# Optimization experiments

Hardware: AMD Instinct MI355X
Metric: run time of the kernel (lower is better)

Reference implementation:

```python
import jax, jax.numpy as jnp
import numpy as np

K_SIGN = 100000.0   # tanh sharpness approximating sign()
EPS = 1e-05         # acos clamp epsilon


def setup_inputs() -> dict:
    key = jax.random.key(0)
    B, N, KV = 2, 8, 64
    contour = jax.random.uniform(key, (B, N, KV, 2), dtype=jnp.float32)  # values in [0,1]
    return {"contour": contour, "size": 128}


def reference(contour, size):
    b, n, kv, _ = contour.shape
    dt = contour.dtype
    # pixel grid, normalized by size (matches torch meshgrid 'ij' + reshape(-1,2)/size)
    g = jnp.arange(size, dtype=dt)
    mesh = jnp.stack(jnp.meshgrid(g, g, indexing="ij"), axis=-1).reshape(-1, 2) / size  # (S2, 2)

    c = contour.reshape(b * n, 1, kv, 2)          # (bn, 1, kv, 2)
    diff = c - mesh[None, :, None, :]             # (bn, S2, kv, 2)
    roll_diff = jnp.roll(diff, -1, axis=2)        # next vertex

    # sign = diff * swap(roll_diff); sign[...,1]-sign[...,0] = d_y*rd_x - d_x*rd_y
    cross = diff[..., 1] * roll_diff[..., 0] - diff[..., 0] * roll_diff[..., 1]
    sign = jnp.tanh(K_SIGN * cross)               # (bn, S2, kv)

    norm_diff = jnp.linalg.norm(diff, axis=3)
    norm_roll = jnp.linalg.norm(roll_diff, axis=3)
    scalar = jnp.sum(diff * roll_diff, axis=3)
    cosang = jnp.clip(scalar / (norm_diff * norm_roll), -1.0 + EPS, 1.0 - EPS)
    angles = jnp.arccos(cosang)                   # (bn, S2, kv)

    sum_angles = jnp.clip(jnp.abs(jnp.sum(sign * angles, axis=2) / (2.0 * jnp.pi)), 0.0, 1.0)
    return sum_angles.reshape(b, n, size, size)
```

## Files before the change

kernel.cpp:

```cpp
#include <hip/hip_runtime.h>
#include <math.h>

#define BLOCK 256
#define SPLIT 4
#define PPT   2
#define MAX_KV_LDS 1024

__device__ __forceinline__ float rcp1(float x)  { return __builtin_amdgcn_rcpf(x); }
__device__ __forceinline__ float rsq1(float x)  { return __builtin_amdgcn_rsqf(x); }
__device__ __forceinline__ float sqrt1(float x) { return __builtin_amdgcn_sqrtf(x); }

__device__ __forceinline__ float edge_term_s(float cr, float dt)
{
    float n2 = fmaf(cr, cr, dt * dt);
    float co = dt * rsq1(n2);
    co = __builtin_amdgcn_fmed3f(co, -0.99999f, 0.99999f);
    float y = fabsf(co);
    float p = fmaf(fmaf(fmaf(-0.0187293f, y, 0.0742610f), y, -0.2121144f),
                   y, 1.5707288f);
    float a = sqrt1(1.0f - y) * p;
    a = (co >= 0.0f) ? a : (3.14159265358979f - a);
    float t  = cr * 100000.0f;
    float s  = t * t;
    float nm = t * fmaf(s + 105.0f, s, 945.0f);
    float qd = fmaf(fmaf(15.0f, s, 420.0f), s, 945.0f);
    float th = __builtin_amdgcn_fmed3f(nm * rcp1(qd), -1.0f, 1.0f);
    return th * a;
}

__global__ __launch_bounds__(BLOCK, 8)
void contour_mask_kernel(const float2* __restrict__ contour,
                         const int* __restrict__ size_ptr,
                         float* __restrict__ out,
                         int out_size, int in0_elems)
{
    __shared__ float2 verts[MAX_KV_LDS + 1];

    const int size     = *size_ptr;
    const int S2       = size * size;
    const int bn_total = out_size / S2;
    const int kv       = in0_elems / (bn_total * 2);

    const int tid  = threadIdx.x;
    const int PIX_PER_BLOCK = (BLOCK / SPLIT) * PPT;
    const int base = blockIdx.x * PIX_PER_BLOCK;

    const int bn0 = base / S2;
    const int rem = base - bn0 * S2;
    const bool one_image = (rem + PIX_PER_BLOCK <= S2) &&
                           (base + PIX_PER_BLOCK <= out_size);
    const bool use_lds = (kv <= MAX_KV_LDS) && one_image;

    if (use_lds) {
        for (int i = tid; i < kv; i += BLOCK)
            verts[i] = contour[(size_t)bn0 * kv + i];
        if (tid == 0)
            verts[kv] = contour[(size_t)bn0 * kv];
    }
    __syncthreads();

    const int seg = tid & (SPLIT - 1);
    const float inv_size = 1.0f / (float)size;
    const float INV2PI = 0.15915494309189535f;

    if (use_lds && kv == 64 && (size & 1) == 0) {
        const int pi0 = rem / size;
        const int pj0 = rem - pi0 * size;
        const int t   = (tid / SPLIT) * PPT;

        int pjA = pj0 + t, piA = pi0;
        while (pjA >= size) { pjA -= size; ++piA; }

        const float mx  = (float)piA * inv_size;
        const float myA = (float)pjA * inv_size;

        const int k0 = seg * 16;
        float2 v = verts[k0];
        float dx  = v.x - mx;
        float dyA = v.y - myA;
        float dyB = dyA - inv_size;
        float accA = 0.0f, accB = 0.0f;

        #pragma unroll
        for (int k = 0; k < 16; ++k) {
            float2 vn = verts[k0 + k + 1];
            float rx  = vn.x - mx;
            float ryA = vn.y - myA;
            float ryB = ryA - inv_size;
            float P   = dx * rx;
            float dtA = fmaf(dyA, ryA, P);
            float dtB = fmaf(dyB, ryB, P);
            float crA = fmaf(dyA, rx, -(dx * ryA));
            float crB = fmaf(dyB, rx, -(dx * ryB));
            accA += edge_term_s(crA, dtA);
            accB += edge_term_s(crB, dtB);
            dx = rx; dyA = ryA; dyB = ryB;
        }

        accA += __shfl_xor(accA, 1, 64);
        accB += __shfl_xor(accB, 1, 64);
        accA += __shfl_xor(accA, 2, 64);
        accB += __shfl_xor(accB, 2, 64);

        if (seg == 0) {
            float2 res;
            res.x = fminf(fabsf(accA) * INV2PI, 1.0f);
            res.y = fminf(fabsf(accB) * INV2PI, 1.0f);
            *(float2*)(out + base + t) = res;
        }
        return;
    }

    const int q  = (kv + SPLIT - 1) / SPLIT;
    const int k0 = min(seg * q, kv);
    const int k1 = min(k0 + q, kv);

    #pragma unroll
    for (int px = 0; px < PPT; ++px) {
        const int pixel = base + (tid / SPLIT) * PPT + px;
        float a = 0.0f;
        if (pixel < out_size && k0 < k1) {
            const int bn = pixel / S2;
            const int p  = pixel - bn * S2;
            const int pi = p / size;
            const int pj = p - pi * size;
            const float mxs = pi * inv_size;
            const float mys = pj * inv_size;
            const float2* vsrc = contour + (size_t)bn * kv;
            float2 v = vsrc[k0];
            float dx = v.x - mxs, dy = v.y - mys;
            for (int k = k0; k < k1; ++k) {
                int kn = k + 1; if (kn == kv) kn = 0;
                float2 vn = vsrc[kn];
                float rx = vn.x - mxs, ry = vn.y - mys;
                float cr = fmaf(dy, rx, -(dx * ry));
                float dt = fmaf(dx, rx, dy * ry);
                a += edge_term_s(cr, dt);
                dx = rx; dy = ry;
            }
        }
        a += __shfl_xor(a, 1, 64);
        a += __shfl_xor(a, 2, 64);
        if (pixel < out_size && seg == 0)
            out[pixel] = fminf(fabsf(a) * INV2PI, 1.0f);
    }
}

extern "C" void kernel_launch(void* const* d_in, const int* in_sizes, int n_in,
                              void* d_out, int out_size, void* d_ws, size_t ws_size,
                              hipStream_t stream)
{
    const float2* contour  = (const float2*)d_in[0];
    const int*    size_ptr = (const int*)d_in[1];
    float*        out      = (float*)d_out;

    const int PIX_PER_BLOCK = (BLOCK / SPLIT) * PPT;
    const int blocks = (out_size + PIX_PER_BLOCK - 1) / PIX_PER_BLOCK;
    contour_mask_kernel<<<blocks, BLOCK, 0, stream>>>(
        contour, size_ptr, out, out_size, in_sizes[0]);
}
```

Before: 69.52 us.

## Replace per-edge acos/tanh with winding-number crossing count plus rare corrections

The fast path no longer evaluates the acos and tanh polynomials for every edge. It accumulates a crossing-based winding number plus cheap clamp-correction terms, which reconstructs the sum of signed angles algebraically. Edges that are nearly collinear with the pixel take a wave-uniform slow branch (rare_fix) that computes the exact clamped term with an atan polynomial. The intent is to cut per-edge transcendental and arithmetic work, at the cost of extra branching and a ballot per iteration, plus numerical-equivalence risk near the clamp thresholds.

New measurement: 75.48 us. 1.09x slower.

```diff
diff --git a/kernel.cpp b/kernel.cpp
--- a/kernel.cpp
+++ b/kernel.cpp
@@ -9,6 +9,56 @@
 __device__ __forceinline__ float rcp1(float x)  { return __builtin_amdgcn_rcpf(x); }
 __device__ __forceinline__ float rsq1(float x)  { return __builtin_amdgcn_rsqf(x); }
 __device__ __forceinline__ float sqrt1(float x) { return __builtin_amdgcn_sqrtf(x); }
+
+#define ACONST 4.4721439e-3f
+#define PIF    3.14159265358979f
+#define PImA   3.1371205f
+#define TWOPI  6.28318530717959f
+#define INV2PI 0.15915494309189535f
+#define K1     2.000040e-5f
+#define CR2MIN 1.6e-9f
+
+__device__ __forceinline__ float rare_fix(float cr, float dt, float c1a)
+{
+    float ac = fabsf(cr), ad = fabsf(dt);
+    float mn = fminf(ac, ad), mx = fmaxf(ac, ad);
+    float q  = mn * rcp1(mx);
+    float s2 = q * q;
+    float r = fmaf(fmaf(fmaf(fmaf(0.0208351f, s2, -0.0851330f), s2,
+                  0.1801410f), s2, -0.3302995f), s2, 0.9998660f) * q;
+    r = (ac > ad) ? (1.57079632679f - r) : r;
+    float theta = (dt < 0.0f) ? (PIF - r) : r;
+    float thc = __builtin_amdgcn_fmed3f(theta, ACONST, PImA);
+    float t  = cr * 100000.0f;
+    float s  = t * t;
+    float nm = t * fmaf(s + 105.0f, s, 945.0f);
+    float qd = fmaf(fmaf(15.0f, s, 420.0f), s, 945.0f);
+    float th = __builtin_amdgcn_fmed3f(nm * rcp1(qd), -1.0f, 1.0f);
+    float scr = (cr >= 0.0f) ? 1.0f : -1.0f;
+    return fmaf(th, thc, -scr * theta) - c1a;
+}
+
+__device__ __forceinline__ void px_step(float rx, float ry, float dx, float P,
+                                        float& dy, bool& dygt, float& W, float& C,
+                                        bool& f2, float& cr_o, float& dt_o, float& c1_o)
+{
+    float cr = fmaf(dy, rx, -(dx * ry));
+    float dt = fmaf(dy, ry, P);
+    bool  rygt = ry > 0.0f;
+    bool  up = (!dygt) && rygt && (cr < 0.0f);
+    bool  dn = dygt && (!rygt) && (cr > 0.0f);
+    W += up ? 1.0f : 0.0f;
+    W -= dn ? 1.0f : 0.0f;
+    float cr2 = cr * cr;
+    float z   = cr * rcp1(dt);
+    float c1  = copysignf(ACONST, z) - z;
+    bool  f1  = cr2 < K1 * (dt * dt);
+    float c1a = f1 ? c1 : 0.0f;
+    C += c1a;
+    f2 = cr2 < CR2MIN;
+    cr_o = cr; dt_o = dt; c1_o = c1a;
+    dy = ry; dygt = rygt;
+}
 
 __device__ __forceinline__ float edge_term_s(float cr, float dt)
 {
@@ -19,7 +69,7 @@
     float p = fmaf(fmaf(fmaf(-0.0187293f, y, 0.0742610f), y, -0.2121144f),
                    y, 1.5707288f);
     float a = sqrt1(1.0f - y) * p;
-    a = (co >= 0.0f) ? a : (3.14159265358979f - a);
+    a = (co >= 0.0f) ? a : (PIF - a);
     float t  = cr * 100000.0f;
     float s  = t * t;
     float nm = t * fmaf(s + 105.0f, s, 945.0f);
@@ -61,7 +111,6 @@
 
     const int seg = tid & (SPLIT - 1);
     const float inv_size = 1.0f / (float)size;
-    const float INV2PI = 0.15915494309189535f;
 
     if (use_lds && kv == 64 && (size & 1) == 0) {
         const int pi0 = rem / size;
@@ -79,7 +128,9 @@
         float dx  = v.x - mx;
         float dyA = v.y - myA;
         float dyB = dyA - inv_size;
-        float accA = 0.0f, accB = 0.0f;
+        bool dygtA = dyA > 0.0f;
+        bool dygtB = dyB > 0.0f;
+        float WA = 0.0f, CA = 0.0f, WB = 0.0f, CB = 0.0f;
 
         #pragma unroll
         for (int k = 0; k < 16; ++k) {
@@ -88,24 +139,28 @@
             float ryA = vn.y - myA;
             float ryB = ryA - inv_size;
             float P   = dx * rx;
-            float dtA = fmaf(dyA, ryA, P);
-            float dtB = fmaf(dyB, ryB, P);
-            float crA = fmaf(dyA, rx, -(dx * ryA));
-            float crB = fmaf(dyB, rx, -(dx * ryB));
-            accA += edge_term_s(crA, dtA);
-            accB += edge_term_s(crB, dtB);
-            dx = rx; dyA = ryA; dyB = ryB;
+            bool f2A, f2B;
+            float crA, dtA, c1A, crB, dtB, c1B;
+            px_step(rx, ryA, dx, P, dyA, dygtA, WA, CA, f2A, crA, dtA, c1A);
+            px_step(rx, ryB, dx, P, dyB, dygtB, WB, CB, f2B, crB, dtB, c1B);
+            if (__ballot(f2A || f2B)) {
+                if (f2A) CA += rare_fix(crA, dtA, c1A);
+                if (f2B) CB += rare_fix(crB, dtB, c1B);
+            }
+            dx = rx;
         }
 
-        accA += __shfl_xor(accA, 1, 64);
-        accB += __shfl_xor(accB, 1, 64);
-        accA += __shfl_xor(accA, 2, 64);
-        accB += __shfl_xor(accB, 2, 64);
+        float SA = fmaf(-TWOPI, WA, CA);
+        float SB = fmaf(-TWOPI, WB, CB);
+        SA += __shfl_xor(SA, 1, 64);
+        SB += __shfl_xor(SB, 1, 64);
+        SA += __shfl_xor(SA, 2, 64);
+        SB += __shfl_xor(SB, 2, 64);
 
         if (seg == 0) {
             float2 res;
-            res.x = fminf(fabsf(accA) * INV2PI, 1.0f);
-            res.y = fminf(fabsf(accB) * INV2PI, 1.0f);
+            res.x = fminf(fabsf(SA) * INV2PI, 1.0f);
+            res.y = fminf(fabsf(SB) * INV2PI, 1.0f);
             *(float2*)(out + base + t) = res;
         }
         return;
```
